# Performance work log

Measured on AMD Instinct MI355X. Metric: run time of the kernel, lower is better.

## Reference

```python
import jax, jax.numpy as jnp
import numpy as np

TAU = 2.0
VTH = 1.0
EPS = 1e-5
T_STEPS = 64

@jax.custom_vjp
def spike_atan(x):
    # Heaviside spike with ATan surrogate gradient (spikingjelly surrogate.ATan, alpha=2.0)
    return (x >= 0.0).astype(x.dtype)

def _spike_fwd(x):
    return spike_atan(x), x

def _spike_bwd(x, g):
    # d/dx [1/pi * atan(pi/2 * alpha * x) + 1/2] with alpha=2 -> 1 / (1 + (pi*x)^2)
    return (g / (1.0 + (jnp.pi * x) ** 2),)

spike_atan.defvjp(_spike_fwd, _spike_bwd)

def bn_eval(x, g, b, m, v):
    return (x - m) * (g / jnp.sqrt(v + EPS)) + b

def setup_inputs() -> dict:
    key = jax.random.key(0)
    ks = jax.random.split(key, 16)
    N, C, L, H, NC = 16384, 22, 63, 64, 4
    D = C * L
    s1 = 1.0 / np.sqrt(D)
    s2 = 1.0 / np.sqrt(H)
    return {
        'x': jax.random.normal(ks[0], (N, C, L), jnp.float32),
        'fc1_w': jax.random.normal(ks[1], (H, D), jnp.float32) * s1,
        'fc1_b': jax.random.normal(ks[2], (H,), jnp.float32) * s1,
        'bn1_g': jax.random.uniform(ks[3], (H,), jnp.float32, 0.5, 1.5),
        'bn1_b': jax.random.normal(ks[4], (H,), jnp.float32) * 0.1,
        'bn1_m': jax.random.normal(ks[5], (H,), jnp.float32) * 0.1,
        'bn1_v': jax.random.uniform(ks[6], (H,), jnp.float32, 0.5, 1.5),
        'fc2_w': jax.random.normal(ks[7], (H, H), jnp.float32) * s2,
        'fc2_b': jax.random.normal(ks[8], (H,), jnp.float32) * s2,
        'bn2_g': jax.random.uniform(ks[9], (H,), jnp.float32, 0.5, 1.5),
        'bn2_b': jax.random.normal(ks[10], (H,), jnp.float32) * 0.1,
        'bn2_m': jax.random.normal(ks[11], (H,), jnp.float32) * 0.1,
        'bn2_v': jax.random.uniform(ks[12], (H,), jnp.float32, 0.5, 1.5),
        'cls_w': jax.random.normal(ks[13], (NC, H), jnp.float32) * s2,
        'cls_b': jax.random.normal(ks[14], (NC,), jnp.float32) * s2,
    }

def reference(x, fc1_w, fc1_b, bn1_g, bn1_b, bn1_m, bn1_v,
              fc2_w, fc2_b, bn2_g, bn2_b, bn2_m, bn2_v, cls_w, cls_b):
    N = x.shape[0]
    x_flat = x.reshape(N, -1)                       # [N, 1386]
    # fc1+bn1 input is identical every timestep -> compute once
    a1 = bn_eval(x_flat @ fc1_w.T + fc1_b, bn1_g, bn1_b, bn1_m, bn1_v)  # [N, 64]

    def step(carry, _):
        v1, v2 = carry
        # LIF 1 (decay_input=True, hard reset to 0)
        h1 = v1 + (a1 - v1) / TAU
        s1 = spike_atan(h1 - VTH)
        v1n = h1 * (1.0 - s1)
        # fc2 + bn2 (eval mode; dropout inactive in inference)
        z = bn_eval(s1 @ fc2_w.T + fc2_b, bn2_g, bn2_b, bn2_m, bn2_v)
        # LIF 2
        h2 = v2 + (z - v2) / TAU
        s2 = spike_atan(h2 - VTH)
        v2n = h2 * (1.0 - s2)
        return (v1n, v2n), s2

    v0 = jnp.zeros_like(a1)
    _, out_seq = jax.lax.scan(step, (v0, v0), None, length=T_STEPS)  # [T, N, 64]
    logits = jnp.einsum('tnh,ch->tnc', out_seq, cls_w) + cls_b        # [T, N, 4]
    return logits.mean(axis=0)                                        # [N, 4]
```

## Files before the change

kernel.cpp:

```cpp
#include <hip/hip_runtime.h>
#include <hip/hip_bf16.h>

#define D_IN 1386
#define EPS 1e-5f
#define CHUNKS 44

typedef __attribute__((ext_vector_type(8))) short short8v;
typedef __attribute__((ext_vector_type(4))) float f32x4;
typedef unsigned short ushortt;

__device__ inline unsigned short bf16rne(float f) {
    unsigned int u = __float_as_uint(f);
    u += 0x7FFFu + ((u >> 16) & 1u);
    return (unsigned short)(u >> 16);
}
__device__ inline float bfbits_to_f(unsigned short b) {
    return __uint_as_float(((unsigned int)b) << 16);
}

union S8U { short8v s; unsigned int u[4]; };

__device__ inline unsigned int cvt2(float v0, float v1, float& r0, float& r1) {
    union { __hip_bfloat162 b2; unsigned int u; } cv;
    cv.b2 = __float22bfloat162_rn(make_float2(v0, v1));
    r0 = v0 - __uint_as_float((cv.u & 0xFFFFu) << 16);
    r1 = v1 - __uint_as_float(cv.u & 0xFFFF0000u);
    return cv.u;
}
__device__ inline unsigned int cvt2n(float v0, float v1) {
    union { __hip_bfloat162 b2; unsigned int u; } cv;
    cv.b2 = __float22bfloat162_rn(make_float2(v0, v1));
    return cv.u;
}

__global__ __launch_bounds__(256) void prep_w3(const float* __restrict__ w,
                                               ushortt* __restrict__ w3) {
    int idx = blockIdx.x * 256 + threadIdx.x;
    if (idx >= CHUNKS * 6144) return;
    int c   = idx / 6144;
    int rem = idx - c * 6144;
    int g   = rem >> 9;
    int l   = (rem >> 3) & 63;
    int j   = rem & 7;
    int T   = g / 3, s = g - 3 * T;
    int h   = 16 * T + (l & 15);
    int k   = 32 * c + 8 * (l >> 4) + j;
    float v = (k < D_IN) ? w[h * D_IN + k] : 0.f;
    unsigned short hh = bf16rne(v);
    float r1 = v - bfbits_to_f(hh);
    unsigned short mm = bf16rne(r1);
    float r2 = r1 - bfbits_to_f(mm);
    unsigned short ll = bf16rne(r2);
    w3[idx] = (s == 0) ? hh : (s == 1) ? mm : ll;
}

__device__ inline void loadA(const float* __restrict__ xrow, int c, int g4,
                             float a[8]) {
    if (c < CHUNKS - 1) {
        const float2* p = (const float2*)(xrow + 32 * c);
#pragma unroll
        for (int i = 0; i < 4; ++i) {
            float2 v = p[i];
            a[2 * i] = v.x; a[2 * i + 1] = v.y;
        }
    } else {
#pragma unroll
        for (int j = 0; j < 8; ++j) {
            int kk = 8 * g4 + j;
            a[j] = (kk < D_IN - 32 * (CHUNKS - 1)) ? xrow[32 * (CHUNKS - 1) + j] : 0.f;
        }
    }
}

__global__ __launch_bounds__(1024, 4) void fc1_mfma(const float* __restrict__ x,
                                                    const ushortt* __restrict__ w3,
                                                    float* __restrict__ y) {
    __shared__ float red[3][4][64][17];
    const int t    = threadIdx.x;
    const int lane = t & 63;
    const int wid  = t >> 6;
    const int kq   = wid >> 2;
    const int sg   = wid & 3;
    const int n0   = blockIdx.x * 64 + sg * 16;
    const int r    = lane & 15;
    const int g4   = lane >> 4;
    const float* xrow = x + (size_t)(n0 + r) * D_IN + 8 * g4;
    const int c0 = 11 * kq;

    f32x4 acc[4];
#pragma unroll
    for (int T = 0; T < 4; ++T) acc[T] = (f32x4){0.f, 0.f, 0.f, 0.f};

    float a0[8], a1p[8], a2p[8];
    loadA(xrow, c0, g4, a0);
    loadA(xrow, c0 + 1, g4, a1p);

#pragma unroll
    for (int i = 0; i < 11; ++i) {
        const int c = c0 + i;
        if (i + 2 < 11) loadA(xrow, c + 2, g4, a2p);
        const short8v* bp = (const short8v*)(w3 + (size_t)c * 6144) + lane;
        short8v B0  = bp[0 * 64],  B1  = bp[1 * 64],  B2  = bp[2 * 64];
        short8v B3  = bp[3 * 64],  B4  = bp[4 * 64],  B5  = bp[5 * 64];
        short8v B6  = bp[6 * 64],  B7  = bp[7 * 64],  B8  = bp[8 * 64];
        short8v B9  = bp[9 * 64],  B10 = bp[10 * 64], B11 = bp[11 * 64];
        S8U Ah, Am, Al;
#pragma unroll
        for (int d = 0; d < 4; ++d) {
            float m0, m1, l0, l1;
            Ah.u[d] = cvt2(a0[2 * d], a0[2 * d + 1], m0, m1);
            Am.u[d] = cvt2(m0, m1, l0, l1);
            Al.u[d] = cvt2n(l0, l1);
        }
        const short8v XH = Ah.s, XM = Am.s, XL = Al.s;
#pragma unroll
        for (int T = 0; T < 4; ++T) {
            const short8v Bh = (T == 0) ? B0 : (T == 1) ? B3 : (T == 2) ? B6 : B9;
            const short8v Bm = (T == 0) ? B1 : (T == 1) ? B4 : (T == 2) ? B7 : B10;
            const short8v Bl = (T == 0) ? B2 : (T == 1) ? B5 : (T == 2) ? B8 : B11;
            f32x4 cacc = acc[T];
            cacc = __builtin_amdgcn_mfma_f32_16x16x32_bf16(XL, Bh, cacc, 0, 0, 0);
            cacc = __builtin_amdgcn_mfma_f32_16x16x32_bf16(XM, Bm, cacc, 0, 0, 0);
            cacc = __builtin_amdgcn_mfma_f32_16x16x32_bf16(XH, Bl, cacc, 0, 0, 0);
            cacc = __builtin_amdgcn_mfma_f32_16x16x32_bf16(XM, Bh, cacc, 0, 0, 0);
            cacc = __builtin_amdgcn_mfma_f32_16x16x32_bf16(XH, Bm, cacc, 0, 0, 0);
            cacc = __builtin_amdgcn_mfma_f32_16x16x32_bf16(XH, Bh, cacc, 0, 0, 0);
            acc[T] = cacc;
        }
#pragma unroll
        for (int j = 0; j < 8; ++j) { a0[j] = a1p[j]; a1p[j] = a2p[j]; }
    }

    if (kq > 0) {
#pragma unroll
        for (int T = 0; T < 4; ++T)
#pragma unroll
            for (int q = 0; q < 4; ++q)
                red[kq - 1][sg][lane][4 * T + q] = acc[T][q];
    }
    __syncthreads();
    if (kq == 0) {
#pragma unroll
        for (int T = 0; T < 4; ++T)
#pragma unroll
            for (int q = 0; q < 4; ++q) {
                float s = acc[T][q]
                        + red[0][sg][lane][4 * T + q]
                        + red[1][sg][lane][4 * T + q]
                        + red[2][sg][lane][4 * T + q];
                y[(size_t)(n0 + 4 * g4 + q) * 64 + 16 * T + r] = s;
            }
    }
}

__global__ __launch_bounds__(256) void snn_kernel(
    const float* __restrict__ y,
    const float* __restrict__ fc1_b,
    const float* __restrict__ bn1_g, const float* __restrict__ bn1_b,
    const float* __restrict__ bn1_m, const float* __restrict__ bn1_v,
    const float* __restrict__ fc2_w, const float* __restrict__ fc2_b,
    const float* __restrict__ bn2_g, const float* __restrict__ bn2_b,
    const float* __restrict__ bn2_m, const float* __restrict__ bn2_v,
    const float* __restrict__ cls_w, const float* __restrict__ cls_b,
    float* __restrict__ out)
{
    const int lane = threadIdx.x & 63;
    const int wid  = threadIdx.x >> 6;
    const int n0   = blockIdx.x * 64 + wid * 16;
    const int r    = lane & 15;
    const int grp  = lane >> 4;

    short8v Whi[4][2], Wlo[4][2];
#pragma unroll
    for (int T = 0; T < 4; ++T) {
        const int hp = 16 * T + r;
        const float scale = bn2_g[hp] / sqrtf(bn2_v[hp] + EPS);
#pragma unroll
        for (int Hh = 0; Hh < 2; ++Hh) {
            S8U hi, lo;
#pragma unroll
            for (int d = 0; d < 4; ++d) {
                const int kk = 32 * Hh + 8 * grp + 2 * d;
                float w0 = fc2_w[hp * 64 + kk]     * scale;
                float w1 = fc2_w[hp * 64 + kk + 1] * scale;
                unsigned short h0 = bf16rne(w0), h1 = bf16rne(w1);
                unsigned short l0 = bf16rne(w0 - bfbits_to_f(h0));
                unsigned short l1 = bf16rne(w1 - bfbits_to_f(h1));
                hi.u[d] = (unsigned int)h0 | ((unsigned int)h1 << 16);
                lo.u[d] = (unsigned int)l0 | ((unsigned int)l1 << 16);
            }
            Whi[T][Hh] = hi.s;
            Wlo[T][Hh] = lo.s;
        }
    }

    float a1[16];
#pragma unroll
    for (int Hh = 0; Hh < 2; ++Hh)
#pragma unroll
        for (int e = 0; e < 8; ++e) {
            const int hin = 32 * Hh + 8 * grp + e;
            float yv = y[(size_t)(n0 + r) * 64 + hin] + fc1_b[hin];
            float s1v = bn1_g[hin] / sqrtf(bn1_v[hin] + EPS);
            a1[Hh * 8 + e] = (yv - bn1_m[hin]) * s1v + bn1_b[hin];
        }

    float biasD[16];
#pragma unroll
    for (int T = 0; T < 4; ++T)
#pragma unroll
        for (int q = 0; q < 4; ++q) {
            const int hp = 16 * T + 4 * grp + q;
            const float scale = bn2_g[hp] / sqrtf(bn2_v[hp] + EPS);
            biasD[4 * T + q] = (fc2_b[hp] - bn2_m[hp]) * scale + bn2_b[hp];
        }

    float v1[16], v2[16], cnt[16];
#pragma unroll
    for (int i = 0; i < 16; ++i) { v1[i] = 0.f; v2[i] = 0.f; cnt[i] = 0.f; }

#pragma unroll 2
    for (int t = 0; t < 64; ++t) {
        S8U s0, s1f;
#pragma unroll
        for (int Hh = 0; Hh < 2; ++Hh)
#pragma unroll
            for (int d = 0; d < 4; ++d) {
                const int i0 = Hh * 8 + 2 * d;
                float h1a = v1[i0]     + (a1[i0]     - v1[i0])     * 0.5f;
                float h1b = v1[i0 + 1] + (a1[i0 + 1] - v1[i0 + 1]) * 0.5f;
                bool sa = h1a >= 1.f, sb = h1b >= 1.f;
                v1[i0]     = sa ? 0.f : h1a;
                v1[i0 + 1] = sb ? 0.f : h1b;
                unsigned int dw = (sa ? 0x3F80u : 0u) | (sb ? 0x3F800000u : 0u);
                if (Hh == 0) s0.u[d] = dw; else s1f.u[d] = dw;
            }
        const short8v S0 = s0.s, S1 = s1f.s;

        f32x4 acc[4];
#pragma unroll
        for (int T = 0; T < 4; ++T) {
            f32x4 c1;
            c1[0] = biasD[4 * T + 0]; c1[1] = biasD[4 * T + 1];
            c1[2] = biasD[4 * T + 2]; c1[3] = biasD[4 * T + 3];
            f32x4 c2 = (f32x4){0.f, 0.f, 0.f, 0.f};
            c1 = __builtin_amdgcn_mfma_f32_16x16x32_bf16(Whi[T][0], S0, c1, 0, 0, 0);
            c2 = __builtin_amdgcn_mfma_f32_16x16x32_bf16(Wlo[T][0], S0, c2, 0, 0, 0);
            c1 = __builtin_amdgcn_mfma_f32_16x16x32_bf16(Whi[T][1], S1, c1, 0, 0, 0);
            c2 = __builtin_amdgcn_mfma_f32_16x16x32_bf16(Wlo[T][1], S1, c2, 0, 0, 0);
            acc[T] = c1 + c2;
        }

#pragma unroll
        for (int T = 0; T < 4; ++T)
#pragma unroll
            for (int q = 0; q < 4; ++q) {
                const int idx = 4 * T + q;
                float z  = acc[T][q];
                float h2 = v2[idx] + (z - v2[idx]) * 0.5f;
                bool s = h2 >= 1.f;
                v2[idx] = s ? 0.f : h2;
                cnt[idx] += s ? 1.f : 0.f;
            }
    }

    float p0 = 0.f, p1 = 0.f, p2 = 0.f, p3 = 0.f;
#pragma unroll
    for (int T = 0; T < 4; ++T)
#pragma unroll
        for (int q = 0; q < 4; ++q) {
            const int hp = 16 * T + 4 * grp + q;
            const float cv = cnt[4 * T + q];
            p0 = fmaf(cv, cls_w[0 * 64 + hp], p0);
            p1 = fmaf(cv, cls_w[1 * 64 + hp], p1);
            p2 = fmaf(cv, cls_w[2 * 64 + hp], p2);
            p3 = fmaf(cv, cls_w[3 * 64 + hp], p3);
        }
    p0 += __shfl_xor(p0, 16); p0 += __shfl_xor(p0, 32);
    p1 += __shfl_xor(p1, 16); p1 += __shfl_xor(p1, 32);
    p2 += __shfl_xor(p2, 16); p2 += __shfl_xor(p2, 32);
    p3 += __shfl_xor(p3, 16); p3 += __shfl_xor(p3, 32);
    if (lane < 16) {
        float4 o;
        o.x = p0 * (1.f / 64.f) + cls_b[0];
        o.y = p1 * (1.f / 64.f) + cls_b[1];
        o.z = p2 * (1.f / 64.f) + cls_b[2];
        o.w = p3 * (1.f / 64.f) + cls_b[3];
        *(float4*)&out[(size_t)(n0 + lane) * 4] = o;
    }
}

extern "C" void kernel_launch(void* const* d_in, const int* in_sizes, int n_in,
                              void* d_out, int out_size, void* d_ws, size_t ws_size,
                              hipStream_t stream) {
    const float* x     = (const float*)d_in[0];
    const float* fc1_w = (const float*)d_in[1];
    const float* fc1_b = (const float*)d_in[2];
    const float* bn1_g = (const float*)d_in[3];
    const float* bn1_b = (const float*)d_in[4];
    const float* bn1_m = (const float*)d_in[5];
    const float* bn1_v = (const float*)d_in[6];
    const float* fc2_w = (const float*)d_in[7];
    const float* fc2_b = (const float*)d_in[8];
    const float* bn2_g = (const float*)d_in[9];
    const float* bn2_b = (const float*)d_in[10];
    const float* bn2_m = (const float*)d_in[11];
    const float* bn2_v = (const float*)d_in[12];
    const float* cls_w = (const float*)d_in[13];
    const float* cls_b = (const float*)d_in[14];

    float*   y  = (float*)d_ws;
    ushortt* w3 = (ushortt*)((char*)d_ws + (4 << 20));

    prep_w3 <<<1056, 256, 0, stream>>>(fc1_w, w3);
    fc1_mfma<<<256, 1024, 0, stream>>>(x, w3, y);
    snn_kernel<<<256, 256, 0, stream>>>(y, fc1_b, bn1_g, bn1_b, bn1_m, bn1_v,
                                        fc2_w, fc2_b, bn2_g, bn2_b, bn2_m, bn2_v,
                                        cls_w, cls_b, (float*)d_out);
}
```

Before: 78.22 us.

## Reuse each weight fragment across two row tiles and double-buffer loads

```diff
diff --git a/kernel.cpp b/kernel.cpp
--- a/kernel.cpp
+++ b/kernel.cpp
@@ -54,89 +54,109 @@
     w3[idx] = (s == 0) ? hh : (s == 1) ? mm : ll;
 }
 
-__device__ inline void loadA(const float* __restrict__ xrow, int c, int g4,
-                             float a[8]) {
-    if (c < CHUNKS - 1) {
-        const float2* p = (const float2*)(xrow + 32 * c);
-#pragma unroll
-        for (int i = 0; i < 4; ++i) {
-            float2 v = p[i];
-            a[2 * i] = v.x; a[2 * i + 1] = v.y;
-        }
-    } else {
-#pragma unroll
-        for (int j = 0; j < 8; ++j) {
-            int kk = 8 * g4 + j;
-            a[j] = (kk < D_IN - 32 * (CHUNKS - 1)) ? xrow[32 * (CHUNKS - 1) + j] : 0.f;
-        }
-    }
-}
-
-__global__ __launch_bounds__(1024, 4) void fc1_mfma(const float* __restrict__ x,
-                                                    const ushortt* __restrict__ w3,
-                                                    float* __restrict__ y) {
-    __shared__ float red[3][4][64][17];
-    const int t    = threadIdx.x;
-    const int lane = t & 63;
-    const int wid  = t >> 6;
-    const int kq   = wid >> 2;
-    const int sg   = wid & 3;
-    const int n0   = blockIdx.x * 64 + sg * 16;
+__global__ __launch_bounds__(256, 2) void fc1_mfma(const float* __restrict__ x,
+                                                   const ushortt* __restrict__ w3,
+                                                   float* __restrict__ y) {
+    __shared__ float red[3][64][33];
+    const int lane = threadIdx.x & 63;
+    const int kq   = threadIdx.x >> 6;
+    const int n0   = blockIdx.x * 32;
     const int r    = lane & 15;
     const int g4   = lane >> 4;
-    const float* xrow = x + (size_t)(n0 + r) * D_IN + 8 * g4;
-    const int c0 = 11 * kq;
-
-    f32x4 acc[4];
-#pragma unroll
-    for (int T = 0; T < 4; ++T) acc[T] = (f32x4){0.f, 0.f, 0.f, 0.f};
-
-    float a0[8], a1p[8], a2p[8];
-    loadA(xrow, c0, g4, a0);
-    loadA(xrow, c0 + 1, g4, a1p);
-
-#pragma unroll
-    for (int i = 0; i < 11; ++i) {
-        const int c = c0 + i;
-        if (i + 2 < 11) loadA(xrow, c + 2, g4, a2p);
+    const float* xA = x + (size_t)(n0 + r) * D_IN + 8 * g4;
+    const float* xB = xA + (size_t)16 * D_IN;
+    const int c0   = 11 * kq;
+
+    f32x4 accA[4], accB[4];
+#pragma unroll
+    for (int T = 0; T < 4; ++T) {
+        accA[T] = (f32x4){0.f, 0.f, 0.f, 0.f};
+        accB[T] = (f32x4){0.f, 0.f, 0.f, 0.f};
+    }
+
+    float aE[16], aO[16];
+    short8v BE[12], BO[12];
+
+    auto loadA32 = [&](int c, float (&a)[16]) {
+        if (c < CHUNKS - 1) {
+            const float2* pA = (const float2*)(xA + 32 * c);
+            const float2* pB = (const float2*)(xB + 32 * c);
+#pragma unroll
+            for (int i = 0; i < 4; ++i) {
+                float2 v = pA[i]; a[2 * i] = v.x; a[2 * i + 1] = v.y;
+                float2 w = pB[i]; a[8 + 2 * i] = w.x; a[8 + 2 * i + 1] = w.y;
+            }
+        } else {
+#pragma unroll
+            for (int j = 0; j < 8; ++j) {
+                int kk = 8 * g4 + j;
+                bool ok = kk < (D_IN - 32 * (CHUNKS - 1));
+                a[j]     = ok ? xA[32 * (CHUNKS - 1) + j] : 0.f;
+                a[8 + j] = ok ? xB[32 * (CHUNKS - 1) + j] : 0.f;
+            }
+        }
+    };
+    auto loadB12 = [&](int c, short8v (&B)[12]) {
         const short8v* bp = (const short8v*)(w3 + (size_t)c * 6144) + lane;
-        short8v B0  = bp[0 * 64],  B1  = bp[1 * 64],  B2  = bp[2 * 64];
-        short8v B3  = bp[3 * 64],  B4  = bp[4 * 64],  B5  = bp[5 * 64];
-        short8v B6  = bp[6 * 64],  B7  = bp[7 * 64],  B8  = bp[8 * 64];
-        short8v B9  = bp[9 * 64],  B10 = bp[10 * 64], B11 = bp[11 * 64];
-        S8U Ah, Am, Al;
+#pragma unroll
+        for (int g = 0; g < 12; ++g) B[g] = bp[g * 64];
+    };
+    auto body = [&](float (&a)[16], short8v (&B)[12]) {
+        S8U Ah0, Am0, Al0, Ah1, Am1, Al1;
 #pragma unroll
         for (int d = 0; d < 4; ++d) {
             float m0, m1, l0, l1;
-            Ah.u[d] = cvt2(a0[2 * d], a0[2 * d + 1], m0, m1);
-            Am.u[d] = cvt2(m0, m1, l0, l1);
-            Al.u[d] = cvt2n(l0, l1);
-        }
-        const short8v XH = Ah.s, XM = Am.s, XL = Al.s;
+            Ah0.u[d] = cvt2(a[2 * d], a[2 * d + 1], m0, m1);
+            Am0.u[d] = cvt2(m0, m1, l0, l1);
+            Al0.u[d] = cvt2n(l0, l1);
+            Ah1.u[d] = cvt2(a[8 + 2 * d], a[8 + 2 * d + 1], m0, m1);
+            Am1.u[d] = cvt2(m0, m1, l0, l1);
+            Al1.u[d] = cvt2n(l0, l1);
+        }
+        const short8v XH0 = Ah0.s, XM0 = Am0.s, XL0 = Al0.s;
+        const short8v XH1 = Ah1.s, XM1 = Am1.s, XL1 = Al1.s;
 #pragma unroll
         for (int T = 0; T < 4; ++T) {
-            const short8v Bh = (T == 0) ? B0 : (T == 1) ? B3 : (T == 2) ? B6 : B9;
-            const short8v Bm = (T == 0) ? B1 : (T == 1) ? B4 : (T == 2) ? B7 : B10;
-            const short8v Bl = (T == 0) ? B2 : (T == 1) ? B5 : (T == 2) ? B8 : B11;
-            f32x4 cacc = acc[T];
-            cacc = __builtin_amdgcn_mfma_f32_16x16x32_bf16(XL, Bh, cacc, 0, 0, 0);
-            cacc = __builtin_amdgcn_mfma_f32_16x16x32_bf16(XM, Bm, cacc, 0, 0, 0);
-            cacc = __builtin_amdgcn_mfma_f32_16x16x32_bf16(XH, Bl, cacc, 0, 0, 0);
-            cacc = __builtin_amdgcn_mfma_f32_16x16x32_bf16(XM, Bh, cacc, 0, 0, 0);
-            cacc = __builtin_amdgcn_mfma_f32_16x16x32_bf16(XH, Bm, cacc, 0, 0, 0);
-            cacc = __builtin_amdgcn_mfma_f32_16x16x32_bf16(XH, Bh, cacc, 0, 0, 0);
-            acc[T] = cacc;
-        }
-#pragma unroll
-        for (int j = 0; j < 8; ++j) { a0[j] = a1p[j]; a1p[j] = a2p[j]; }
-    }
+            const short8v Bh = B[3 * T], Bm = B[3 * T + 1], Bl = B[3 * T + 2];
+            f32x4 c1 = accA[T];
+            c1 = __builtin_amdgcn_mfma_f32_16x16x32_bf16(XL0, Bh, c1, 0, 0, 0);
+            c1 = __builtin_amdgcn_mfma_f32_16x16x32_bf16(XM0, Bm, c1, 0, 0, 0);
+            c1 = __builtin_amdgcn_mfma_f32_16x16x32_bf16(XH0, Bl, c1, 0, 0, 0);
+            c1 = __builtin_amdgcn_mfma_f32_16x16x32_bf16(XM0, Bh, c1, 0, 0, 0);
+            c1 = __builtin_amdgcn_mfma_f32_16x16x32_bf16(XH0, Bm, c1, 0, 0, 0);
+            c1 = __builtin_amdgcn_mfma_f32_16x16x32_bf16(XH0, Bh, c1, 0, 0, 0);
+            accA[T] = c1;
+            f32x4 c2 = accB[T];
+            c2 = __builtin_amdgcn_mfma_f32_16x16x32_bf16(XL1, Bh, c2, 0, 0, 0);
+            c2 = __builtin_amdgcn_mfma_f32_16x16x32_bf16(XM1, Bm, c2, 0, 0, 0);
+            c2 = __builtin_amdgcn_mfma_f32_16x16x32_bf16(XH1, Bl, c2, 0, 0, 0);
+            c2 = __builtin_amdgcn_mfma_f32_16x16x32_bf16(XM1, Bh, c2, 0, 0, 0);
+            c2 = __builtin_amdgcn_mfma_f32_16x16x32_bf16(XH1, Bm, c2, 0, 0, 0);
+            c2 = __builtin_amdgcn_mfma_f32_16x16x32_bf16(XH1, Bh, c2, 0, 0, 0);
+            accB[T] = c2;
+        }
+    };
+
+    loadA32(c0, aE);     loadB12(c0, BE);
+    loadA32(c0 + 1, aO); loadB12(c0 + 1, BO);
+
+#pragma unroll
+    for (int j = 0; j < 5; ++j) {
+        body(aE, BE);
+        if (2 * j + 2 < 11) { loadA32(c0 + 2 * j + 2, aE); loadB12(c0 + 2 * j + 2, BE); }
+        body(aO, BO);
+        if (2 * j + 3 < 11) { loadA32(c0 + 2 * j + 3, aO); loadB12(c0 + 2 * j + 3, BO); }
+    }
+    body(aE, BE);
 
     if (kq > 0) {
 #pragma unroll
         for (int T = 0; T < 4; ++T)
 #pragma unroll
-            for (int q = 0; q < 4; ++q)
-                red[kq - 1][sg][lane][4 * T + q] = acc[T][q];
+            for (int q = 0; q < 4; ++q) {
+                red[kq - 1][lane][4 * T + q]      = accA[T][q];
+                red[kq - 1][lane][16 + 4 * T + q] = accB[T][q];
+            }
     }
     __syncthreads();
     if (kq == 0) {
@@ -144,11 +164,12 @@
         for (int T = 0; T < 4; ++T)
 #pragma unroll
             for (int q = 0; q < 4; ++q) {
-                float s = acc[T][q]
-                        + red[0][sg][lane][4 * T + q]
-                        + red[1][sg][lane][4 * T + q]
-                        + red[2][sg][lane][4 * T + q];
-                y[(size_t)(n0 + 4 * g4 + q) * 64 + 16 * T + r] = s;
+                float sA = accA[T][q] + red[0][lane][4 * T + q]
+                         + red[1][lane][4 * T + q] + red[2][lane][4 * T + q];
+                float sB = accB[T][q] + red[0][lane][16 + 4 * T + q]
+                         + red[1][lane][16 + 4 * T + q] + red[2][lane][16 + 4 * T + q];
+                y[(size_t)(n0 + 4 * g4 + q) * 64 + 16 * T + r] = sA;
+                y[(size_t)(n0 + 16 + 4 * g4 + q) * 64 + 16 * T + r] = sB;
             }
     }
 }
@@ -313,7 +334,7 @@
     ushortt* w3 = (ushortt*)((char*)d_ws + (4 << 20));
 
     prep_w3 <<<1056, 256, 0, stream>>>(fc1_w, w3);
-    fc1_mfma<<<256, 1024, 0, stream>>>(x, w3, y);
+    fc1_mfma<<<512,  256, 0, stream>>>(x, w3, y);
     snn_kernel<<<256, 256, 0, stream>>>(y, fc1_b, bn1_g, bn1_b, bn1_m, bn1_v,
                                         fc2_w, fc2_b, bn2_g, bn2_b, bn2_m, bn2_v,
                                         cls_w, cls_b, (float*)d_out);
```

New measurement: 75.58 us. -3.4%, faster.
